# Performance work log

Hardware: AMD Instinct MI355X
Metric: run time of the kernel (lower is better)

## Reference

```python
import jax, jax.numpy as jnp
import numpy as np

N_HEADS = 16
MASK_NEG = -1e32


def setup_inputs() -> dict:
    key = jax.random.key(0)
    k0, k1, k2, k3, k4 = jax.random.split(key, 5)
    B, S, D = 8, 1024, 1024
    return {
        "q": jax.random.normal(k0, (B, S, D), dtype=jnp.float32),
        "k": jax.random.normal(k1, (B, S, D), dtype=jnp.float32),
        "v1": jax.random.normal(k2, (B, S, D), dtype=jnp.float32),
        "v2": jax.random.normal(k3, (B, S, D), dtype=jnp.float32),
        "counter_attention_mask": jax.random.randint(k4, (B, S), 0, 2, dtype=jnp.int32),
    }


def reference(q, k, v1, v2, counter_attention_mask):
    B, S, D = q.shape
    H = N_HEADS
    dk = D // H

    def split_heads(x):
        return x.reshape(B, S, H, dk).transpose(0, 2, 1, 3)  # [B,H,S,dk]

    qh, kh, v1h, v2h = split_heads(q), split_heads(k), split_heads(v1), split_heads(v2)

    # scaled dot-product scores [B,H,S,S]
    scores = jnp.einsum("bhqd,bhkd->bhqk", qh, kh) / jnp.sqrt(jnp.float32(dk))

    # create_mask(input, 0): allowed only where key_idx < query_idx (strict causal)
    i = jnp.arange(S)[:, None]
    j = jnp.arange(S)[None, :]
    allowed = j < i  # [S,S]
    scores = jnp.where(allowed[None, None], scores, MASK_NEG)

    # first softmax
    p = jax.nn.softmax(scores, axis=-1)

    # counter-attention mask: zero out masked key columns (per batch, all heads/rows)
    cm = counter_attention_mask[:, None, None, :]  # [B,1,1,S]
    p = jnp.where(cm == 1, jnp.float32(0.0), p)

    # second softmax over the (partially zeroed) probabilities
    p = jax.nn.softmax(p, axis=-1)

    # zero the first query row (pad_zero concat in the original)
    p = p.at[:, :, 0, :].set(0.0)

    out1 = jnp.einsum("bhqk,bhkd->bhqd", p, v1h)
    out2 = jnp.einsum("bhqk,bhkd->bhqd", p, v2h)

    def merge_heads(x):
        return x.transpose(0, 2, 1, 3).reshape(B, S, D)

    return merge_heads(out1), merge_heads(out2)
```

## Files before the change

kernel.cpp:

```cpp
#include <hip/hip_runtime.h>
#include <hip/hip_bf16.h>

#define B_ 8
#define S_ 1024
#define D_ 1024
#define H_ 16
#define DK_ 64
#define BH_ (B_ * H_)
#define NQ 8
#define QTASK 256
#define NPERS 768

typedef float f32x4 __attribute__((ext_vector_type(4)));
typedef short s16x8 __attribute__((ext_vector_type(8)));
typedef short s16x4 __attribute__((ext_vector_type(4)));

#define EXP2F(x) __builtin_amdgcn_exp2f(x)
#define LOG2E 1.44269504088896f

static __device__ __forceinline__ short f2b(float f) {
  unsigned u = __builtin_bit_cast(unsigned, f);
  u = u + 0x7FFFu + ((u >> 16) & 1u);
  return (short)(u >> 16);
}
static __device__ __forceinline__ short f2bn(float f) {
  __hip_bfloat16 h = __float2bfloat16(f);
  return __builtin_bit_cast(short, h);
}

static __device__ __forceinline__ int slotf(int g, int e) {
  return (e < 4) ? (4 * g + e) : (16 + 4 * g + (e - 4));
}


__global__ __launch_bounds__(256) void prep_k(const float* __restrict__ k,
                                              short* __restrict__ kb) {
  const int bid = blockIdx.x;
  const int s0 = (bid & 63) * 16;
  const int b = bid >> 6;
  const int tid = threadIdx.x;
#pragma unroll
  for (int it = 0; it < 8; ++it) {
    int li = it * 256 + tid;
    int s = s0 + (li >> 7);
    int ch = li & 127;
    int h = ch >> 3;
    int dk0 = (ch & 7) * 8;
    const float* src = k + ((size_t)(b * S_ + s)) * D_ + ch * 8;
    s16x8 o;
#pragma unroll
    for (int e = 0; e < 8; ++e) o[e] = f2b(src[e]);
    *(s16x8*)(kb + ((size_t)((b * H_ + h) * S_ + s)) * DK_ + dk0) = o;
  }
}

__global__ __launch_bounds__(256) void prep_v(const float* __restrict__ v1,
                                              const float* __restrict__ v2,
                                              short* __restrict__ v1f,
                                              short* __restrict__ v2f,
                                              float* __restrict__ vs) {
  const int bid = blockIdx.x;
  const int sg = bid & 3;
  const int h = (bid >> 2) & 15;
  const int b = bid >> 6;
  const int tid = threadIdx.x;
  const int db = tid >> 6;
  const int lane = tid & 63;
  const int r = lane & 15;
  const int g = lane >> 4;
  const size_t inbase = (size_t)b * S_ * D_ + h * DK_ + db * 16 + r;
  float s1 = 0.f, s2 = 0.f;
#pragma unroll
  for (int it = 0; it < 8; ++it) {
    int jt = sg * 8 + it;
    int j0 = jt * 32;
    s16x8 o1, o2;
#pragma unroll
    for (int e = 0; e < 8; ++e) {
      int j = j0 + slotf(g, e);
      float a = v1[inbase + (size_t)j * D_];
      float c = v2[inbase + (size_t)j * D_];
      s1 += a;
      s2 += c;
      o1[e] = f2b(a);
      o2[e] = f2b(c);
    }
    size_t off = (((size_t)((b * H_ + h) * 32 + jt) * 4 + db) * 64 + lane) * 8;
    *(s16x8*)(v1f + off) = o1;
    *(s16x8*)(v2f + off) = o2;
  }
  s1 += __shfl_xor(s1, 16);
  s1 += __shfl_xor(s1, 32);
  s2 += __shfl_xor(s2, 16);
  s2 += __shfl_xor(s2, 32);
  if (g == 0) {
    int dd = db * 16 + r;
    atomicAdd(&vs[(size_t)b * D_ + h * DK_ + dd], s1);
    atomicAdd(&vs[(size_t)(B_ + b) * D_ + h * DK_ + dd], s2);
  }
}

__global__ __launch_bounds__(256, 3) void attn_series2q(
    const float* __restrict__ q, const short* __restrict__ kb,
    const short* __restrict__ v1f, const short* __restrict__ v2f,
    const int* __restrict__ cm, const float* __restrict__ vs,
    unsigned* __restrict__ counters, float* __restrict__ out) {
  const int tid = threadIdx.x;
  const int wid = tid >> 6;
  const int lane = tid & 63;
  const int r = lane & 15;
  const int g = lane >> 4;

  unsigned xcc = 0;
  asm volatile("s_getreg_b32 %0, hwreg(HW_REG_XCC_ID)" : "=s"(xcc));
  const int xq = (int)(xcc & 7u);

  __shared__ __align__(16) char sbuf[2][12288];
  __shared__ unsigned cmw[32];
  __shared__ int taskS;

  const int srow = tid >> 3;
  const int sch = tid & 7;

#define SLK(reg, jtv) reg = *(const s16x8*)(kbh + (size_t)(jtv)*2048 + tid * 8);
#define SLV(d1, d2, jtv)                                           \
  {                                                                \
    d1 = *(const s16x8*)(v1bh + (size_t)(jtv)*2048 + tid * 8);     \
    d2 = *(const s16x8*)(v2bh + (size_t)(jtv)*2048 + tid * 8);     \
  }
#define SWK(buf, reg) \
  *(s16x8*)((buf) + srow * 128 + ((sch ^ (srow & 7)) * 16)) = reg;
#define SWV(buf, d1, d2)                        \
  {                                             \
    *(s16x8*)((buf) + 4096 + tid * 16) = d1;    \
    *(s16x8*)((buf) + 8192 + tid * 16) = d2;    \
  }
#define KFRAG(sK, row, quad) \
  (*(const s16x8*)((sK) + (row)*128 + (((quad) ^ ((row)&7)) * 16)))

  float* out1 = out;
  float* out2 = out + (size_t)B_ * S_ * D_;

  for (int qi = 0; qi < NQ; ++qi) {
    const int qq = (xq + qi) & 7;
    for (;;) {
      __syncthreads();
      if (tid == 0) taskS = (int)atomicAdd(&counters[qq * 64], 1u);
      __syncthreads();
      const int task = taskS;
      if (task >= QTASK) break;

      const int seg = 15 - (task >> 4);
      const int bh = (task & 15) * 8 + qq;
      const int b = bh >> 4, h = bh & 15;

      const int qw = seg * 64 + wid * 16;
      const int iq = qw + r;
      const int njt = 2 * seg + 2;

      {
        const int* cmb = cm + b * S_;
#pragma unroll
        for (int it = 0; it < 4; ++it) {
          unsigned long long m = __ballot(cmb[it * 256 + tid] == 1);
          if (lane == 0) {
            int w0 = it * 8 + wid * 2;
            cmw[w0] = (unsigned)m;
            cmw[w0 + 1] = (unsigned)(m >> 32);
          }
        }
      }

      const float qscale = 0.125f * LOG2E;
      s16x8 qf0, qf1;
      {
        const float* qp = q + ((size_t)(b * S_ + qw + r)) * D_ + h * DK_;
#pragma unroll
        for (int e = 0; e < 8; ++e) qf0[e] = f2bn(qp[8 * g + e] * qscale);
#pragma unroll
        for (int e = 0; e < 8; ++e) qf1[e] = f2bn(qp[32 + 8 * g + e] * qscale);
      }

      const short* kbh = kb + (size_t)bh * S_ * DK_;
      const short* v1bh = v1f + (size_t)bh * 32 * 2048;
      const short* v2bh = v2f + (size_t)bh * 32 * 2048;

      f32x4 a11[4], a12[4], a21[4], a22[4];
#pragma unroll
      for (int d0 = 0; d0 < 4; ++d0) {
        a11[d0] = (f32x4){0.f, 0.f, 0.f, 0.f};
        a12[d0] = (f32x4){0.f, 0.f, 0.f, 0.f};
        a21[d0] = (f32x4){0.f, 0.f, 0.f, 0.f};
        a22[d0] = (f32x4){0.f, 0.f, 0.f, 0.f};
      }
      float Z1 = 0.f, T1 = 0.f, T2 = 0.f;

      {
        s16x8 rk, rv1, rv2;
        SLK(rk, 0);
        SLV(rv1, rv2, 0);
        SWK(sbuf[0], rk);
        SWV(sbuf[0], rv1, rv2);
        __syncthreads();
        for (int jt = 0; jt < njt; ++jt) {
          const int jb = jt * 32;
          const char* sB = sbuf[jt & 1];
          const bool pf = (jt + 1 < njt);
          s16x8 rk2, rv12, rv22;
          if (pf) {
            SLK(rk2, jt + 1);
            SLV(rv12, rv22, jt + 1);
          }
          if (jb < qw + 16) {
            s16x8 k00 = KFRAG(sB, r, g);
            s16x8 k01 = KFRAG(sB, r, 4 + g);
            s16x8 k10 = KFRAG(sB, 16 + r, g);
            s16x8 k11 = KFRAG(sB, 16 + r, 4 + g);
            f32x4 s0 = {0.f, 0.f, 0.f, 0.f}, s1 = {0.f, 0.f, 0.f, 0.f};
            s0 = __builtin_amdgcn_mfma_f32_16x16x32_bf16(k00, qf0, s0, 0, 0, 0);
            s0 = __builtin_amdgcn_mfma_f32_16x16x32_bf16(k01, qf1, s0, 0, 0, 0);
            s1 = __builtin_amdgcn_mfma_f32_16x16x32_bf16(k10, qf0, s1, 0, 0, 0);
            s1 = __builtin_amdgcn_mfma_f32_16x16x32_bf16(k11, qf1, s1, 0, 0, 0);
            const unsigned cw = cmw[jt];
            const bool cb = (jb + 32 > qw);
            float w1[8], w2[8];
#pragma unroll
            for (int s2 = 0; s2 < 2; ++s2) {
              f32x4 sv = s2 ? s1 : s0;
#pragma unroll
              for (int e = 0; e < 4; ++e) {
                int sl = s2 * 16 + 4 * g + e;
                int j = jb + sl;
                float pe = EXP2F(sv[e]);
                if (cb) pe = (j < iq) ? pe : 0.f;
                Z1 += pe;
                float pm = ((cw >> sl) & 1u) ? 0.f : pe;
                float pm2 = pm * pm;
                T1 += pm;
                T2 += pm2;
                int o = s2 * 4 + e;
                w1[o] = pm;
                w2[o] = pm2;
              }
            }
            s16x8 wa1, wa2;
#pragma unroll
            for (int e = 0; e < 8; ++e) {
              wa1[e] = f2bn(w1[e]);
              wa2[e] = f2bn(w2[e]);
            }
            s16x8 vb1[4], vb2[4];
#pragma unroll
            for (int db = 0; db < 4; ++db) {
              vb1[db] = *(const s16x8*)(sB + 4096 + (db * 64 + lane) * 16);
              vb2[db] = *(const s16x8*)(sB + 8192 + (db * 64 + lane) * 16);
            }
#pragma unroll
            for (int db = 0; db < 4; ++db) {
              a11[db] = __builtin_amdgcn_mfma_f32_16x16x32_bf16(wa1, vb1[db], a11[db], 0, 0, 0);
              a21[db] = __builtin_amdgcn_mfma_f32_16x16x32_bf16(wa1, vb2[db], a21[db], 0, 0, 0);
              a12[db] = __builtin_amdgcn_mfma_f32_16x16x32_bf16(wa2, vb1[db], a12[db], 0, 0, 0);
              a22[db] = __builtin_amdgcn_mfma_f32_16x16x32_bf16(wa2, vb2[db], a22[db], 0, 0, 0);
            }
          }
          if (pf) {
            SWK(sbuf[(jt + 1) & 1], rk2);
            SWV(sbuf[(jt + 1) & 1], rv12, rv22);
          }
          __syncthreads();
        }
      }

      Z1 += __shfl_xor(Z1, 16);
      Z1 += __shfl_xor(Z1, 32);
      T1 += __shfl_xor(T1, 16);
      T1 += __shfl_xor(T1, 32);
      T2 += __shfl_xor(T2, 16);
      T2 += __shfl_xor(T2, 32);

      const float iz = (Z1 > 0.f) ? (1.f / Z1) : 0.f;
      const float f1 = iz;
      const float f2 = 0.5f * iz * iz;
      const float Z2 = (float)S_ + T1 * f1 + T2 * f2;
      const float izz = 1.f / Z2;
      const float g1v = f1 * izz;
      const float g2v = f2 * izz;
      const float gcv = izz;

      const float* vs1 = vs + (size_t)b * D_ + h * DK_;
      const float* vs2 = vs + (size_t)(B_ + b) * D_ + h * DK_;

#pragma unroll
      for (int e = 0; e < 4; ++e) {
        float gg1 = __shfl(g1v, 4 * g + e);
        float gg2 = __shfl(g2v, 4 * g + e);
        float ggc = __shfl(gcv, 4 * g + e);
        int io = qw + 4 * g + e;
        bool zero = (io == 0);
        size_t ro = ((size_t)(b * S_) + io) * D_ + h * DK_;
#pragma unroll
        for (int db = 0; db < 4; ++db) {
          int dd = db * 16 + r;
          float o1 = a11[db][e] * gg1 + a12[db][e] * gg2 + vs1[dd] * ggc;
          float o2 = a21[db][e] * gg1 + a22[db][e] * gg2 + vs2[dd] * ggc;
          out1[ro + dd] = zero ? 0.f : o1;
          out2[ro + dd] = zero ? 0.f : o2;
        }
      }
    }
  }
#undef SLK
#undef SLV
#undef SWK
#undef SWV
#undef KFRAG
}


__global__ __launch_bounds__(256) void vsum_kernel(const float* __restrict__ v1,
                                                   const float* __restrict__ v2,
                                                   float* __restrict__ vs) {
  int bid = blockIdx.x;
  int sc = bid & 7, dc = (bid >> 3) & 3, b = bid >> 5;
  int d = dc * 256 + threadIdx.x;
  const float* p1 = v1 + ((size_t)b * S_ + sc * 128) * D_ + d;
  const float* p2 = v2 + ((size_t)b * S_ + sc * 128) * D_ + d;
  float s1 = 0.f, s2 = 0.f;
  for (int j = 0; j < 128; ++j) {
    s1 += p1[(size_t)j * D_];
    s2 += p2[(size_t)j * D_];
  }
  atomicAdd(&vs[b * D_ + d], s1);
  atomicAdd(&vs[B_ * D_ + b * D_ + d], s2);
}

__global__ __launch_bounds__(256) void dualattn_fallback(
    const float* __restrict__ q, const float* __restrict__ k,
    const float* __restrict__ v1, const float* __restrict__ v2,
    const int* __restrict__ cm, const float* __restrict__ vs,
    float* __restrict__ out) {
  const int bid = blockIdx.x;
  const int qt = bid & 15;
  const int h = (bid >> 4) & 15;
  const int b = bid >> 8;
  const int tid = threadIdx.x;
  const int wid = tid >> 6;
  const int lane = tid & 63;
  const int r = lane & 15;
  const int g = lane >> 4;
  const int qw = qt * 64 + wid * 16;
  const int iq = qw + r;

  __shared__ __align__(16) char kbuf[32 * 128];
  __shared__ __align__(16) char vtb1[64 * 64];
  __shared__ __align__(16) char vtb2[64 * 64];
  __shared__ unsigned cmw[32];

  {
    const int* cmb = cm + b * S_;
#pragma unroll
    for (int it = 0; it < 4; ++it) {
      int c = cmb[it * 256 + tid];
      unsigned long long m = __ballot(c == 1);
      if (lane == 0) {
        int w0 = (it * 256 + wid * 64) >> 5;
        cmw[w0] = (unsigned)m;
        cmw[w0 + 1] = (unsigned)(m >> 32);
      }
    }
  }

  s16x8 qf0, qf1;
  {
    const float* qp = q + ((size_t)(b * S_) + qw + r) * D_ + h * DK_;
#pragma unroll
    for (int e = 0; e < 8; ++e) qf0[e] = f2b(qp[8 * g + e] * 0.125f);
#pragma unroll
    for (int e = 0; e < 8; ++e) qf1[e] = f2b(qp[32 + 8 * g + e] * 0.125f);
  }

  const int njt = 2 * qt + 2;
  const float* kbase = k + (size_t)(b * S_) * D_ + h * DK_;
  const float* v1base = v1 + (size_t)(b * S_) * D_ + h * DK_;
  const float* v2base = v2 + (size_t)(b * S_) * D_ + h * DK_;
  const int srow = tid >> 3;
  const int sch = tid & 7;

  float m1 = -INFINITY, Z1 = 0.f;
  for (int jt = 0; jt < njt; ++jt) {
    const int jbase = jt * 32;
    __syncthreads();
    {
      const float* kr = kbase + (size_t)(jbase + srow) * D_ + sch * 8;
      s16x8 pk;
#pragma unroll
      for (int e = 0; e < 8; ++e) pk[e] = f2b(kr[e]);
      *(s16x8*)(kbuf + srow * 128 + ((sch ^ (srow & 7)) * 16)) = pk;
    }
    __syncthreads();
    if (jbase < qw + 16) {
#pragma unroll
      for (int sub = 0; sub < 2; ++sub) {
        const int jsb = jbase + sub * 16;
        if (jsb < qw + 16) {
          const int row = sub * 16 + r;
          s16x8 ka0 = *(const s16x8*)(kbuf + row * 128 + ((g ^ (row & 7)) * 16));
          s16x8 ka1 = *(const s16x8*)(kbuf + row * 128 + (((4 + g) ^ (row & 7)) * 16));
          f32x4 sv = {0.f, 0.f, 0.f, 0.f};
          sv = __builtin_amdgcn_mfma_f32_16x16x32_bf16(ka0, qf0, sv, 0, 0, 0);
          sv = __builtin_amdgcn_mfma_f32_16x16x32_bf16(ka1, qf1, sv, 0, 0, 0);
          float tm = m1;
#pragma unroll
          for (int e = 0; e < 4; ++e) {
            int j = jsb + 4 * g + e;
            if (j < iq) tm = fmaxf(tm, sv[e]);
          }
          if (tm > m1) { Z1 *= __expf(m1 - tm); m1 = tm; }
#pragma unroll
          for (int e = 0; e < 4; ++e) {
            int j = jsb + 4 * g + e;
            if (j < iq) Z1 += __expf(sv[e] - tm);
          }
        }
      }
    }
  }
#pragma unroll
  for (int off = 16; off < 64; off <<= 1) {
    float mo = __shfl_xor(m1, off);
    float zo = __shfl_xor(Z1, off);
    float mn = fmaxf(m1, mo);
    if (mn > -INFINITY) {
      Z1 = Z1 * __expf(m1 - mn) + zo * __expf(mo - mn);
      m1 = mn;
    }
  }
  float z1i;
  if (m1 > -INFINITY) { z1i = 1.f / Z1; }
  else { z1i = 0.f; m1 = 0.f; }

  f32x4 acc1[4], acc2[4];
#pragma unroll
  for (int d0 = 0; d0 < 4; ++d0) {
    acc1[d0] = (f32x4){0.f, 0.f, 0.f, 0.f};
    acc2[d0] = (f32x4){0.f, 0.f, 0.f, 0.f};
  }
  float wsum = 0.f;

  for (int jt = 0; jt < njt; ++jt) {
    const int jbase = jt * 32;
    __syncthreads();
    {
      const float* kr = kbase + (size_t)(jbase + srow) * D_ + sch * 8;
      s16x8 pk;
#pragma unroll
      for (int e = 0; e < 8; ++e) pk[e] = f2b(kr[e]);
      *(s16x8*)(kbuf + srow * 128 + ((sch ^ (srow & 7)) * 16)) = pk;
      const float* v1r = v1base + (size_t)(jbase + srow) * D_ + sch * 8;
      const float* v2r = v2base + (size_t)(jbase + srow) * D_ + sch * 8;
#pragma unroll
      for (int e = 0; e < 8; ++e) {
        int dd = sch * 8 + e;
        int off = dd * 64 + (((srow >> 2) ^ (dd & 7)) * 8) + (srow & 3) * 2;
        *(short*)(vtb1 + off) = f2b(v1r[e]);
        *(short*)(vtb2 + off) = f2b(v2r[e]);
      }
    }
    __syncthreads();
    if (jbase < qw + 16) {
      const unsigned cmword = cmw[jbase >> 5];
      float w[8];
#pragma unroll
      for (int sub = 0; sub < 2; ++sub) {
        const int jsb = jbase + sub * 16;
        if (jsb < qw + 16) {
          const int row = sub * 16 + r;
          s16x8 ka0 = *(const s16x8*)(kbuf + row * 128 + ((g ^ (row & 7)) * 16));
          s16x8 ka1 = *(const s16x8*)(kbuf + row * 128 + (((4 + g) ^ (row & 7)) * 16));
          f32x4 sv = {0.f, 0.f, 0.f, 0.f};
          sv = __builtin_amdgcn_mfma_f32_16x16x32_bf16(ka0, qf0, sv, 0, 0, 0);
          sv = __builtin_amdgcn_mfma_f32_16x16x32_bf16(ka1, qf1, sv, 0, 0, 0);
#pragma unroll
          for (int e = 0; e < 4; ++e) {
            int j = jsb + 4 * g + e;
            float x = 0.f;
            if (j < iq && !((cmword >> (j & 31)) & 1u)) {
              float p = __expf(sv[e] - m1) * z1i;
              x = __expf(p) - 1.f;
            }
            w[sub * 4 + e] = x;
            wsum += x;
          }
        } else {
#pragma unroll
          for (int e = 0; e < 4; ++e) w[sub * 4 + e] = 0.f;
        }
      }
      s16x8 wa;
#pragma unroll
      for (int e = 0; e < 8; ++e) wa[e] = f2b(w[e]);
#pragma unroll
      for (int db = 0; db < 4; ++db) {
        const int dd = db * 16 + r;
        const int off0 = dd * 64 + ((g ^ (dd & 7)) * 8);
        const int off1 = dd * 64 + (((4 + g) ^ (dd & 7)) * 8);
        s16x4 lo1 = *(const s16x4*)(vtb1 + off0);
        s16x4 hi1 = *(const s16x4*)(vtb1 + off1);
        s16x8 vb1 = __builtin_shufflevector(lo1, hi1, 0, 1, 2, 3, 4, 5, 6, 7);
        acc1[db] = __builtin_amdgcn_mfma_f32_16x16x32_bf16(wa, vb1, acc1[db], 0, 0, 0);
        s16x4 lo2 = *(const s16x4*)(vtb2 + off0);
        s16x4 hi2 = *(const s16x4*)(vtb2 + off1);
        s16x8 vb2 = __builtin_shufflevector(lo2, hi2, 0, 1, 2, 3, 4, 5, 6, 7);
        acc2[db] = __builtin_amdgcn_mfma_f32_16x16x32_bf16(wa, vb2, acc2[db], 0, 0, 0);
      }
    }
  }

  wsum += __shfl_xor(wsum, 16);
  wsum += __shfl_xor(wsum, 32);
  const float z2 = (float)S_ + wsum;

  float* out1 = out;
  float* out2 = out + (size_t)B_ * S_ * D_;
#pragma unroll
  for (int e = 0; e < 4; ++e) {
    float z2e = __shfl(z2, 4 * g + e);
    float inv = 1.f / z2e;
    int io = qw + 4 * g + e;
    bool zero = (io == 0);
    size_t ro = ((size_t)(b * S_) + io) * D_ + h * DK_;
#pragma unroll
    for (int db = 0; db < 4; ++db) {
      int dd = db * 16 + r;
      float c1 = vs[(size_t)b * D_ + h * DK_ + dd];
      float c2 = vs[(size_t)(B_ + b) * D_ + h * DK_ + dd];
      out1[ro + dd] = zero ? 0.f : (acc1[db][e] + c1) * inv;
      out2[ro + dd] = zero ? 0.f : (acc2[db][e] + c2) * inv;
    }
  }
}


extern "C" void kernel_launch(void* const* d_in, const int* in_sizes, int n_in,
                              void* d_out, int out_size, void* d_ws, size_t ws_size,
                              hipStream_t stream) {
  (void)in_sizes; (void)n_in; (void)out_size;
  const float* q = (const float*)d_in[0];
  const float* k = (const float*)d_in[1];
  const float* v1 = (const float*)d_in[2];
  const float* v2 = (const float*)d_in[3];
  const int* cm = (const int*)d_in[4];
  float* outp = (float*)d_out;

  const size_t VS_BYTES = 2 * B_ * D_ * sizeof(float);
  const size_t CTR_BYTES = NQ * 64 * sizeof(unsigned);
  const size_t FRAG_SHORTS = (size_t)BH_ * S_ * DK_;
  const size_t FRAG_BYTES = FRAG_SHORTS * 2;
  const size_t NEED = VS_BYTES + CTR_BYTES + 3 * FRAG_BYTES;

  float* vs = (float*)d_ws;
  (void)hipMemsetAsync(d_ws, 0, VS_BYTES + CTR_BYTES, stream);

  if (ws_size >= NEED) {
    unsigned* counters = (unsigned*)((char*)d_ws + VS_BYTES);
    short* kb = (short*)((char*)d_ws + VS_BYTES + CTR_BYTES);
    short* v1f = kb + FRAG_SHORTS;
    short* v2f = v1f + FRAG_SHORTS;
    prep_k<<<B_ * (S_ / 16), 256, 0, stream>>>(k, kb);
    prep_v<<<B_ * H_ * 4, 256, 0, stream>>>(v1, v2, v1f, v2f, vs);
    attn_series2q<<<NPERS, 256, 0, stream>>>(q, kb, v1f, v2f, cm, vs, counters,
                                             outp);
  } else {
    vsum_kernel<<<256, 256, 0, stream>>>(v1, v2, vs);
    dualattn_fallback<<<B_ * H_ * 16, 256, 0, stream>>>(q, k, v1, v2, cm, vs, outp);
  }
}
```

Measured before the change: 106.9 us.

## Fold counter mask into V prep and compute row sums via MFMA

The counter-attention mask is now applied once, in the V preprocessing kernel, by zeroing the masked key rows of the bf16 V fragments. The attention loop therefore feeds unmasked exp weights to the PV MFMAs. The per-row normaliser sums (Z, T1, T2) are no longer accumulated as scalar adds with shuffle reductions; three extra MFMAs per tile against an all-ones vector and a per-lane mask vector produce them. This removes per-element mask selects, scalar accumulation and the cross-lane reductions, at the cost of three more MFMAs per tile and sums computed from bf16-rounded weights.

Result: faster. 102.0 us (-4.6%).

```diff
diff --git a/kernel.cpp b/kernel.cpp
--- a/kernel.cpp
+++ b/kernel.cpp
@@ -56,6 +56,7 @@
 
 __global__ __launch_bounds__(256) void prep_v(const float* __restrict__ v1,
                                               const float* __restrict__ v2,
+                                              const int* __restrict__ cm,
                                               short* __restrict__ v1f,
                                               short* __restrict__ v2f,
                                               float* __restrict__ vs) {
@@ -69,6 +70,7 @@
   const int r = lane & 15;
   const int g = lane >> 4;
   const size_t inbase = (size_t)b * S_ * D_ + h * DK_ + db * 16 + r;
+  const int* cmb = cm + b * S_;
   float s1 = 0.f, s2 = 0.f;
 #pragma unroll
   for (int it = 0; it < 8; ++it) {
@@ -82,8 +84,9 @@
       float c = v2[inbase + (size_t)j * D_];
       s1 += a;
       s2 += c;
-      o1[e] = f2b(a);
-      o2[e] = f2b(c);
+      bool msk = (cmb[j] == 1);
+      o1[e] = msk ? (short)0 : f2b(a);
+      o2[e] = msk ? (short)0 : f2b(c);
     }
     size_t off = (((size_t)((b * H_ + h) * 32 + jt) * 4 + db) * 64 + lane) * 8;
     *(s16x8*)(v1f + off) = o1;
@@ -100,7 +103,7 @@
   }
 }
 
-__global__ __launch_bounds__(256, 3) void attn_series2q(
+__global__ __launch_bounds__(256, 3) void attn_series2s(
     const float* __restrict__ q, const short* __restrict__ kb,
     const short* __restrict__ v1f, const short* __restrict__ v2f,
     const int* __restrict__ cm, const float* __restrict__ vs,
@@ -138,6 +141,10 @@
 #define KFRAG(sK, row, quad) \
   (*(const s16x8*)((sK) + (row)*128 + (((quad) ^ ((row)&7)) * 16)))
 
+  s16x8 ones;
+#pragma unroll
+  for (int e = 0; e < 8; ++e) ones[e] = (short)0x3F80;
+
   float* out1 = out;
   float* out2 = out + (size_t)B_ * S_ * D_;
 
@@ -193,7 +200,9 @@
         a21[d0] = (f32x4){0.f, 0.f, 0.f, 0.f};
         a22[d0] = (f32x4){0.f, 0.f, 0.f, 0.f};
       }
-      float Z1 = 0.f, T1 = 0.f, T2 = 0.f;
+      f32x4 za = {0.f, 0.f, 0.f, 0.f};
+      f32x4 t1a = {0.f, 0.f, 0.f, 0.f};
+      f32x4 t2a = {0.f, 0.f, 0.f, 0.f};
 
       {
         s16x8 rk, rv1, rv2;
@@ -229,25 +238,23 @@
               f32x4 sv = s2 ? s1 : s0;
 #pragma unroll
               for (int e = 0; e < 4; ++e) {
-                int sl = s2 * 16 + 4 * g + e;
-                int j = jb + sl;
                 float pe = EXP2F(sv[e]);
-                if (cb) pe = (j < iq) ? pe : 0.f;
-                Z1 += pe;
-                float pm = ((cw >> sl) & 1u) ? 0.f : pe;
-                float pm2 = pm * pm;
-                T1 += pm;
-                T2 += pm2;
+                if (cb) {
+                  int j = jb + s2 * 16 + 4 * g + e;
+                  pe = (j < iq) ? pe : 0.f;
+                }
                 int o = s2 * 4 + e;
-                w1[o] = pm;
-                w2[o] = pm2;
+                w1[o] = pe;
+                w2[o] = pe * pe;
               }
             }
-            s16x8 wa1, wa2;
-#pragma unroll
-            for (int e = 0; e < 8; ++e) {
-              wa1[e] = f2bn(w1[e]);
-              wa2[e] = f2bn(w2[e]);
+            s16x8 wa1, wa2, mf;
+#pragma unroll
+            for (int o = 0; o < 8; ++o) {
+              wa1[o] = f2bn(w1[o]);
+              wa2[o] = f2bn(w2[o]);
+              int kk = slotf(g, o);
+              mf[o] = ((cw >> kk) & 1u) ? (short)0 : (short)0x3F80;
             }
             s16x8 vb1[4], vb2[4];
 #pragma unroll
@@ -262,6 +269,9 @@
               a12[db] = __builtin_amdgcn_mfma_f32_16x16x32_bf16(wa2, vb1[db], a12[db], 0, 0, 0);
               a22[db] = __builtin_amdgcn_mfma_f32_16x16x32_bf16(wa2, vb2[db], a22[db], 0, 0, 0);
             }
+            za = __builtin_amdgcn_mfma_f32_16x16x32_bf16(wa1, ones, za, 0, 0, 0);
+            t1a = __builtin_amdgcn_mfma_f32_16x16x32_bf16(wa1, mf, t1a, 0, 0, 0);
+            t2a = __builtin_amdgcn_mfma_f32_16x16x32_bf16(wa2, mf, t2a, 0, 0, 0);
           }
           if (pf) {
             SWK(sbuf[(jt + 1) & 1], rk2);
@@ -271,30 +281,19 @@
         }
       }
 
-      Z1 += __shfl_xor(Z1, 16);
-      Z1 += __shfl_xor(Z1, 32);
-      T1 += __shfl_xor(T1, 16);
-      T1 += __shfl_xor(T1, 32);
-      T2 += __shfl_xor(T2, 16);
-      T2 += __shfl_xor(T2, 32);
-
-      const float iz = (Z1 > 0.f) ? (1.f / Z1) : 0.f;
-      const float f1 = iz;
-      const float f2 = 0.5f * iz * iz;
-      const float Z2 = (float)S_ + T1 * f1 + T2 * f2;
-      const float izz = 1.f / Z2;
-      const float g1v = f1 * izz;
-      const float g2v = f2 * izz;
-      const float gcv = izz;
-
       const float* vs1 = vs + (size_t)b * D_ + h * DK_;
       const float* vs2 = vs + (size_t)(B_ + b) * D_ + h * DK_;
 
 #pragma unroll
       for (int e = 0; e < 4; ++e) {
-        float gg1 = __shfl(g1v, 4 * g + e);
-        float gg2 = __shfl(g2v, 4 * g + e);
-        float ggc = __shfl(gcv, 4 * g + e);
+        const float iz = (za[e] > 0.f) ? (1.f / za[e]) : 0.f;
+        const float f1 = iz;
+        const float f2v = 0.5f * iz * iz;
+        const float Z2 = (float)S_ + t1a[e] * f1 + t2a[e] * f2v;
+        const float izz = 1.f / Z2;
+        const float gg1 = f1 * izz;
+        const float gg2 = f2v * izz;
+        const float ggc = izz;
         int io = qw + 4 * g + e;
         bool zero = (io == 0);
         size_t ro = ((size_t)(b * S_) + io) * D_ + h * DK_;
@@ -567,8 +566,8 @@
     short* v1f = kb + FRAG_SHORTS;
     short* v2f = v1f + FRAG_SHORTS;
     prep_k<<<B_ * (S_ / 16), 256, 0, stream>>>(k, kb);
-    prep_v<<<B_ * H_ * 4, 256, 0, stream>>>(v1, v2, v1f, v2f, vs);
-    attn_series2q<<<NPERS, 256, 0, stream>>>(q, kb, v1f, v2f, cm, vs, counters,
+    prep_v<<<B_ * H_ * 4, 256, 0, stream>>>(v1, v2, cm, v1f, v2f, vs);
+    attn_series2s<<<NPERS, 256, 0, stream>>>(q, kb, v1f, v2f, cm, vs, counters,
                                              outp);
   } else {
     vsum_kernel<<<256, 256, 0, stream>>>(v1, v2, vs);
```
